# Performance work log

Hardware: AMD Instinct MI355X
Metric: run time of the kernel (lower is better)

Reference implementation:

```python
import jax, jax.numpy as jnp
import numpy as np

B, N, F_IN, H, OUT = 64, 1024, 195, 128, 64
K1, K2 = N // 2, N // 4  # ceil(0.5*N), ceil(0.5*K1)
EPS = 1e-5


def setup_inputs() -> dict:
    key = jax.random.key(0)
    ks = jax.random.split(key, 16)
    rn = lambda k, s: jax.random.normal(k, s, dtype=jnp.float32) * 0.1
    inp = {
        "input": jax.random.normal(ks[0], (B, N, F_IN), dtype=jnp.float32),
        # SAGEConv1 (195->128): lin_l (neighbors, w/ bias), lin_r (root, no bias)
        "W1l": rn(ks[1], (H, F_IN)), "b1l": jnp.zeros((H,), jnp.float32),
        "W1r": rn(ks[2], (H, F_IN)),
        # SAGPooling1 GNN = GraphConv(128->1): lin_rel (sum aggr, w/ bias), lin_root (no bias)
        "Wp1_rel": rn(ks[3], (1, H)), "bp1_rel": jnp.zeros((1,), jnp.float32),
        "Wp1_root": rn(ks[4], (1, H)),
        # SAGEConv2 (128->64)
        "W2l": rn(ks[5], (OUT, H)), "b2l": jnp.zeros((OUT,), jnp.float32),
        "W2r": rn(ks[6], (OUT, H)),
        # SAGPooling2 GNN = GraphConv(64->1)
        "Wp2_rel": rn(ks[7], (1, OUT)), "bp2_rel": jnp.zeros((1,), jnp.float32),
        "Wp2_root": rn(ks[8], (1, OUT)),
        # MLP head
        "fc1_w": rn(ks[9], (512, OUT)), "fc1_b": jnp.zeros((512,), jnp.float32),
        "bn1_g": jnp.ones((512,), jnp.float32), "bn1_b": jnp.zeros((512,), jnp.float32),
        "bn1_m": jnp.zeros((512,), jnp.float32), "bn1_v": jnp.ones((512,), jnp.float32),
        "fc2_w": rn(ks[10], (256, 512)), "fc2_b": jnp.zeros((256,), jnp.float32),
        "bn2_g": jnp.ones((256,), jnp.float32), "bn2_b": jnp.zeros((256,), jnp.float32),
        "bn2_m": jnp.zeros((256,), jnp.float32), "bn2_v": jnp.ones((256,), jnp.float32),
        "fc3_w": rn(ks[11], (2, 256)), "fc3_b": jnp.zeros((2,), jnp.float32),
    }
    return inp


def _corr_adj(x):
    # Pearson corrcoef over rows of x [B,N,F] -> boolean adjacency [B,N,N] (corr > 0.5)
    xc = x - x.mean(axis=-1, keepdims=True)
    cov = jnp.einsum("bnf,bmf->bnm", xc, xc)
    d = jnp.sqrt(jnp.clip(jnp.einsum("bnnf->bn", cov[..., None] * 0 + 0) + jnp.diagonal(cov, axis1=1, axis2=2), 1e-12))
    corr = cov / (d[:, :, None] * d[:, None, :])
    return (corr > 0.5).astype(x.dtype)  # symmetric, includes self-loops


def _sage(x, A, Wl, bl, Wr):
    # PyG SAGEConv: lin_l(mean_{j in N(i)} x_j) + lin_r(x_i)
    deg = A.sum(axis=-1, keepdims=True)
    agg = jnp.einsum("bnm,bmf->bnf", A, x) / jnp.maximum(deg, 1.0)
    return jnp.einsum("bnf,hf->bnh", agg, Wl) + bl + jnp.einsum("bnf,hf->bnh", x, Wr)


def _sagpool(x, A, Wrel, brel, Wroot, k):
    # score via GraphConv (sum aggr): lin_rel(sum_j x_j) + lin_root(x_i)
    agg = jnp.einsum("bnm,bmf->bnf", A, x)
    score = (jnp.einsum("bnf,of->bno", agg, Wrel) + brel
             + jnp.einsum("bnf,of->bno", x, Wroot))[..., 0]  # [B,N]
    top_s, idx = jax.lax.top_k(score, k)  # per-graph top-k nodes
    x_new = jnp.take_along_axis(x, idx[:, :, None], axis=1) * jnp.tanh(top_s)[:, :, None]
    A_new = jnp.take_along_axis(A, idx[:, :, None], axis=1)
    A_new = jnp.take_along_axis(A_new, idx[:, None, :], axis=2)
    return x_new, A_new


def _bn_eval(x, g, b, m, v):
    return g * (x - m) * jax.lax.rsqrt(v + EPS) + b


def reference(input, W1l, b1l, W1r, Wp1_rel, bp1_rel, Wp1_root,
              W2l, b2l, W2r, Wp2_rel, bp2_rel, Wp2_root,
              fc1_w, fc1_b, bn1_g, bn1_b, bn1_m, bn1_v,
              fc2_w, fc2_b, bn2_g, bn2_b, bn2_m, bn2_v,
              fc3_w, fc3_b):
    A = _corr_adj(input)                                   # [B,N,N]
    x = jax.nn.relu(_sage(input, A, W1l, b1l, W1r))        # [B,N,128]
    x, A = _sagpool(x, A, Wp1_rel, bp1_rel, Wp1_root, K1)  # [B,K1,128]
    x = jax.nn.relu(_sage(x, A, W2l, b2l, W2r))            # [B,K1,64]
    x, A = _sagpool(x, A, Wp2_rel, bp2_rel, Wp2_root, K2)  # [B,K2,64]
    x = x.mean(axis=1)                                     # global mean pool -> [B,64]
    x = _bn_eval(jax.nn.relu(x @ fc1_w.T + fc1_b), bn1_g, bn1_b, bn1_m, bn1_v)
    x = _bn_eval(jax.nn.relu(x @ fc2_w.T + fc2_b), bn2_g, bn2_b, bn2_m, bn2_v)
    x = x @ fc3_w.T + fc3_b
    return jax.nn.softmax(x, axis=1)
```

## Files before the change

### kernel.cpp

```cpp
#include <hip/hip_runtime.h>
#include <cstdint>


typedef __bf16 bf16x8 __attribute__((ext_vector_type(8)));
typedef float  floatx4 __attribute__((ext_vector_type(4)));

#define MFMA_BF16(a, b, c) __builtin_amdgcn_mfma_f32_16x16x32_bf16((a), (b), (c), 0, 0, 0)

static constexpr int BATCH = 64, NNODE = 1024, FIN = 195, FPAD = 224;
static constexpr int HD = 128, OD = 64, KP1 = 512, KP2 = 256;

static constexpr size_t OFF_GHI   = 0;
static constexpr size_t OFF_GLO   = 8388608;
static constexpr size_t OFF_A1B   = 16777216;
static constexpr size_t OFF_YR2   = 18874368;
static constexpr size_t OFF_X2    = 35651584;
static constexpr size_t OFF_XHI   = 0;
static constexpr size_t OFF_XLO   = 29360128;
static constexpr size_t OFF_ABITS = 58720256;
static constexpr size_t OFF_X1    = 67108864;
static constexpr size_t OFF_P1    = 100663296;
static constexpr size_t OFF_Q1    = OFF_P1 + 262144;
static constexpr size_t OFF_S1    = OFF_Q1 + 262144;
static constexpr size_t OFF_IDX1  = OFF_S1 + 262144;
static constexpr size_t OFF_GATE1 = OFF_IDX1 + 131072;
static constexpr size_t OFF_P2    = OFF_GATE1 + 131072;
static constexpr size_t OFF_Q2    = OFF_P2 + 131072;
static constexpr size_t OFF_S2    = OFF_Q2 + 131072;
static constexpr size_t OFF_IDX2  = OFF_S2 + 131072;
static constexpr size_t OFF_GATE2 = OFF_IDX2 + 65536;
static constexpr size_t OFF_W1HI  = OFF_GATE2 + 65536;
static constexpr size_t OFF_W1LO  = OFF_W1HI + 114688;
static constexpr size_t OFF_W2HI  = OFF_W1LO + 114688;
static constexpr size_t OFF_W2LO  = OFF_W2HI + 32768;
static constexpr size_t OFF_XHAT  = 102760448;
static constexpr size_t OFF_YR1   = 102760448;

__global__ __launch_bounds__(256) void prep_pack_kernel(
    const float* __restrict__ x, __bf16* __restrict__ xhi,
    __bf16* __restrict__ xlo, __bf16* __restrict__ xhat,
    const float* __restrict__ W1l, const float* __restrict__ W1r,
    __bf16* __restrict__ hi1, __bf16* __restrict__ lo1,
    const float* __restrict__ W2l, const float* __restrict__ W2r,
    __bf16* __restrict__ hi2, __bf16* __restrict__ lo2) {
  int bid = blockIdx.x;
  if (bid < 16384) {
    int row  = bid * 4 + (threadIdx.x >> 6);
    int lane = threadIdx.x & 63;
    const float* xr = x + (long)row * FIN;
    int k0 = lane * 4;
    float v[4];
#pragma unroll
    for (int i = 0; i < 4; ++i) v[i] = (k0 + i < FIN) ? xr[k0 + i] : 0.f;
    float s = v[0] + v[1] + v[2] + v[3];
#pragma unroll
    for (int o = 32; o; o >>= 1) s += __shfl_xor(s, o);
    float mean = s * (1.f / (float)FIN);
    float c[4], ss = 0.f;
#pragma unroll
    for (int i = 0; i < 4; ++i) {
      c[i] = (k0 + i < FIN) ? (v[i] - mean) : 0.f;
      ss += c[i] * c[i];
    }
#pragma unroll
    for (int o = 32; o; o >>= 1) ss += __shfl_xor(ss, o);
    float inv = rsqrtf(fmaxf(ss, 1e-12f));
    if (k0 < FPAD) {
      __bf16 hi4[4], lo4[4], hat4[4];
#pragma unroll
      for (int i = 0; i < 4; ++i) {
        float xv = (k0 + i < FIN) ? v[i] : 0.f;
        __bf16 h = (__bf16)xv;
        hi4[i] = h;
        lo4[i] = (__bf16)(xv - (float)h);
        hat4[i] = (__bf16)(c[i] * inv);
      }
      long base = (long)row * FPAD + k0;
      *(uint2*)&xhi[base]  = *(const uint2*)hi4;
      *(uint2*)&xlo[base]  = *(const uint2*)lo4;
      *(uint2*)&xhat[base] = *(const uint2*)hat4;
    }
  } else if (bid < 16384 + 224) {
    int idx = (bid - 16384) * 256 + threadIdx.x;
    int h = idx / FPAD, k = idx % FPAD;
    float v = 0.f;
    if (k < FIN) v = (h < HD) ? W1l[h * FIN + k] : W1r[(h - HD) * FIN + k];
    __bf16 a = (__bf16)v;
    hi1[idx] = a;
    lo1[idx] = (__bf16)(v - (float)a);
  } else {
    int idx = (bid - 16384 - 224) * 256 + threadIdx.x;
    int h = idx / HD, k = idx % HD;
    float v = (h < OD) ? W2l[h * HD + k] : W2r[(h - OD) * HD + k];
    __bf16 a = (__bf16)v;
    hi2[idx] = a;
    lo2[idx] = (__bf16)(v - (float)a);
  }
}

static constexpr int CK = 40;
__global__ __launch_bounds__(256) void corr_kernel(
    const __bf16* __restrict__ xhat, unsigned short* __restrict__ Abits) {
  __shared__ __align__(16) __bf16 sI[128 * CK];
  __shared__ __align__(16) __bf16 sJ[128 * CK];
  int bid = blockIdx.x;
  int xcd = bid & 7;
  int m = bid >> 3;
  int b = xcd + ((m & 7) << 3);
  int rem = m >> 3, bi = 0;
  while (rem >= 8 - bi) { rem -= 8 - bi; ++bi; }
  int bj = bi + rem;
  int i0 = bi * 128, j0 = bj * 128;
  const __bf16* Xb = xhat + (long)b * NNODE * FPAD;
  int lane = threadIdx.x & 63, wave = threadIdx.x >> 6;
  int wi = (wave >> 1) * 64, wj = (wave & 1) * 64;
  int lr = lane & 15, lk = (lane >> 4) * 8;
  int strow = threadIdx.x & 127;
  int stc = (threadIdx.x >> 7) * 8;
  floatx4 zero = {0.f, 0.f, 0.f, 0.f};
  floatx4 acc[4][4];
#pragma unroll
  for (int i = 0; i < 4; ++i)
#pragma unroll
    for (int j = 0; j < 4; ++j) acc[i][j] = zero;
  for (int kk = 0; kk < 7; ++kk) {
    int k0 = kk * 32;
    __syncthreads();
    {
      const __bf16* gI = Xb + (long)(i0 + strow) * FPAD + k0;
      const __bf16* gJ = Xb + (long)(j0 + strow) * FPAD + k0;
      *(uint4*)&sI[strow * CK + stc]      = *(const uint4*)(gI + stc);
      *(uint4*)&sI[strow * CK + stc + 16] = *(const uint4*)(gI + stc + 16);
      *(uint4*)&sJ[strow * CK + stc]      = *(const uint4*)(gJ + stc);
      *(uint4*)&sJ[strow * CK + stc + 16] = *(const uint4*)(gJ + stc + 16);
    }
    __syncthreads();
    bf16x8 af[4], bf[4];
#pragma unroll
    for (int t = 0; t < 4; ++t) {
      af[t] = *(const bf16x8*)&sI[(wi + t * 16 + lr) * CK + lk];
      bf[t] = *(const bf16x8*)&sJ[(wj + t * 16 + lr) * CK + lk];
    }
#pragma unroll
    for (int ti = 0; ti < 4; ++ti)
#pragma unroll
      for (int tj = 0; tj < 4; ++tj)
        acc[ti][tj] = MFMA_BF16(af[ti], bf[tj], acc[ti][tj]);
  }
#pragma unroll
  for (int ti = 0; ti < 4; ++ti)
#pragma unroll
    for (int tj = 0; tj < 4; ++tj) {
      floatx4 a = acc[ti][tj];
      unsigned long long m0 = __ballot(a[0] > 0.5f);
      unsigned long long m1 = __ballot(a[1] > 0.5f);
      unsigned long long m2 = __ballot(a[2] > 0.5f);
      unsigned long long m3 = __ballot(a[3] > 0.5f);
      if (lane < 16) {
        unsigned long long mm = (lane & 2) ? ((lane & 1) ? m3 : m2)
                                           : ((lane & 1) ? m1 : m0);
        unsigned short piece = (unsigned short)(mm >> ((lane >> 2) * 16));
        int grow = i0 + wi + ti * 16 + lane;
        int gcol = (j0 + wj + tj * 16) >> 4;
        Abits[((long)b * NNODE + grow) * 64 + gcol] = piece;
      }
    }
}

template <int K, int NCOL>
__global__ __launch_bounds__(256, 2) void gemm_split_kernel(
    const __bf16* __restrict__ Ahi, const __bf16* __restrict__ Alo,
    const __bf16* __restrict__ Bhi, const __bf16* __restrict__ Blo,
    float* __restrict__ C, int mblocks,
    unsigned long long* __restrict__ A64, int ntrans) {
  constexpr int ldc = NCOL * 128;
  int bid = blockIdx.x;
  if (bid >= mblocks * NCOL) {
    int t = bid - mblocks * NCOL;
    if (t >= ntrans) return;
    int b = t / 28, pi = t % 28;
    int rem = pi, rb = 1;
    while (rem >= rb) { rem -= rb; ++rb; }
    int cb = rem;
    int wave = threadIdx.x >> 6, lane = threadIdx.x & 63;
    int dr = rb * 2 + (wave >> 1);
    int dc = cb * 2 + (wave & 1);
    long base = (long)b * NNODE;
    unsigned long long xv = A64[(base + dc * 64 + lane) * 16 + dr];
    const unsigned long long M1  = 0x5555555555555555ULL;
    const unsigned long long M2  = 0x3333333333333333ULL;
    const unsigned long long M4  = 0x0F0F0F0F0F0F0F0FULL;
    const unsigned long long M8  = 0x00FF00FF00FF00FFULL;
    const unsigned long long M16 = 0x0000FFFF0000FFFFULL;
    const unsigned long long M32 = 0x00000000FFFFFFFFULL;
#define TSTEP(Kk, M)                                                      \
    {                                                                     \
      unsigned long long y = __shfl_xor(xv, Kk);                          \
      xv = ((lane & Kk) == 0) ? ((xv & (M)) | ((y & (M)) << Kk))          \
                              : ((xv & ~(M)) | ((y & ~(M)) >> Kk));       \
    }
    TSTEP(1, M1) TSTEP(2, M2) TSTEP(4, M4) TSTEP(8, M8) TSTEP(16, M16) TSTEP(32, M32)
#undef TSTEP
    A64[(base + dr * 64 + lane) * 16 + dc] = xv;
    return;
  }
  int mrow, col;
  if (NCOL == 2) {
    int xcd = bid & 7;
    int q = bid >> 3;
    col = q & 1;
    mrow = (xcd << 6) + (q >> 1);
  } else {
    mrow = bid;
    col = 0;
  }
  long row0 = (long)mrow * 128;
  int col0 = col * 128;
  int lane = threadIdx.x & 63, wave = threadIdx.x >> 6;
  int wi = (wave >> 1) * 64, wj = (wave & 1) * 64;
  int lr = lane & 15, lk = (lane >> 4) * 8;
  const __bf16* pAh = Ahi + (row0 + wi + lr) * (long)K + lk;
  const __bf16* pAl = Alo + (row0 + wi + lr) * (long)K + lk;
  const __bf16* pBh = Bhi + (long)(col0 + wj + lr) * K + lk;
  const __bf16* pBl = Blo + (long)(col0 + wj + lr) * K + lk;
  floatx4 zero = {0.f, 0.f, 0.f, 0.f};
  floatx4 acc[4][4];
#pragma unroll
  for (int i = 0; i < 4; ++i)
#pragma unroll
    for (int j = 0; j < 4; ++j) acc[i][j] = zero;
#pragma unroll
  for (int kk = 0; kk < (K >> 5); ++kk) {
    int k0 = kk * 32;
    bf16x8 ah[4], al[4], bh[4], bl[4];
#pragma unroll
    for (int t = 0; t < 4; ++t) {
      ah[t] = *(const bf16x8*)(pAh + (long)t * 16 * K + k0);
      al[t] = *(const bf16x8*)(pAl + (long)t * 16 * K + k0);
      bh[t] = *(const bf16x8*)(pBh + (long)t * 16 * K + k0);
      bl[t] = *(const bf16x8*)(pBl + (long)t * 16 * K + k0);
    }
#pragma unroll
    for (int tj = 0; tj < 4; ++tj)
#pragma unroll
      for (int ti = 0; ti < 4; ++ti) {
        acc[ti][tj] = MFMA_BF16(ah[ti], bh[tj], acc[ti][tj]);
        acc[ti][tj] = MFMA_BF16(ah[ti], bl[tj], acc[ti][tj]);
        acc[ti][tj] = MFMA_BF16(al[ti], bh[tj], acc[ti][tj]);
      }
  }
#pragma unroll
  for (int ti = 0; ti < 4; ++ti)
#pragma unroll
    for (int tj = 0; tj < 4; ++tj)
#pragma unroll
      for (int rr = 0; rr < 4; ++rr) {
        long grow = row0 + wi + ti * 16 + (lane >> 4) * 4 + rr;
        int gcol = col0 + wj + tj * 16 + (lane & 15);
        C[grow * ldc + gcol] = acc[ti][tj][rr];
      }
}

__global__ __launch_bounds__(256) void sage1_kernel(
    const unsigned int* __restrict__ Abits32, const float* __restrict__ YR1,
    const float* __restrict__ b1l, const float* __restrict__ Wrel,
    const float* __restrict__ Wroot, float* __restrict__ x1,
    float* __restrict__ p1, float* __restrict__ q1) {
  int half = threadIdx.x >> 7;
  int node = blockIdx.x * 2 + half;
  int b = node >> 10;
  int h = threadIdx.x & 127;
  __shared__ int list[2][1024];
  __shared__ int s_deg[2];
  __shared__ float redp[2][2], redq[2][2];
  if (h < 32) {
    unsigned int word = Abits32[(long)node * 32 + h];
    int cnt = __popc(word);
    int off = cnt;
#pragma unroll
    for (int o = 1; o < 32; o <<= 1) {
      int v = __shfl_up(off, o);
      if (h >= o) off += v;
    }
    off -= cnt;
    if (h == 31) s_deg[half] = off + cnt;
    int basei = h * 32;
    while (word) {
      int t = __ffs(word) - 1;
      word &= word - 1;
      list[half][off++] = basei + t;
    }
  }
  __syncthreads();
  int deg = s_deg[half];
  long ybase = (long)(b << 10) * 256;
  float accv = 0.f;
  for (int d = 0; d < deg; ++d)
    accv += YR1[ybase + (long)list[half][d] * 256 + h];
  float R = YR1[(long)node * 256 + 128 + h];
  float v = accv / (float)(deg < 1 ? 1 : deg) + b1l[h] + R;
  v = fmaxf(v, 0.f);
  x1[(long)node * 128 + h] = v;
  float pv = v * Wrel[h], qv = v * Wroot[h];
#pragma unroll
  for (int o = 32; o; o >>= 1) { pv += __shfl_xor(pv, o); qv += __shfl_xor(qv, o); }
  int wv = h >> 6, lane = h & 63;
  if (lane == 0) { redp[half][wv] = pv; redq[half][wv] = qv; }
  __syncthreads();
  if (h == 0) {
    p1[node] = redp[half][0] + redp[half][1];
    q1[node] = redq[half][0] + redq[half][1];
  }
}

__global__ __launch_bounds__(256) void score_kernel(
    const unsigned int* __restrict__ bits32, const float* __restrict__ p,
    const float* __restrict__ q, const float* __restrict__ brel,
    float* __restrict__ score, int nwords, int rpb_shift) {
  int row = blockIdx.x * 4 + (threadIdx.x >> 6);
  int lane = threadIdx.x & 63;
  int b = row >> rpb_shift;
  const unsigned int* wptr = bits32 + (long)row * nwords;
  const float* pb = p + ((long)b << rpb_shift);
  float s = 0.f;
  if (lane < nwords) {
    unsigned int word = wptr[lane];
    while (word) {
      int t = __ffs(word) - 1;
      word &= word - 1;
      s += pb[lane * 32 + t];
    }
  }
#pragma unroll
  for (int o = 32; o; o >>= 1) s += __shfl_xor(s, o);
  if (lane == 0) score[row] = s + q[row] + brel[0];
}

__global__ void topk_kernel(const float* __restrict__ score, int n, int k,
                            int* __restrict__ idx_out, float* __restrict__ gate_out) {
  int b = blockIdx.x, tid = threadIdx.x;
  float s = score[b * n + tid];
  unsigned int fb = __float_as_uint(s);
  unsigned int key = (fb & 0x80000000u) ? ~fb : (fb | 0x80000000u);
  __shared__ int hist[256];
  __shared__ unsigned int sh_prefix;
  __shared__ int sh_target, cnt_gt, cnt_eq, outpos;
  if (tid == 0) { sh_prefix = 0; sh_target = k; cnt_gt = 0; cnt_eq = 0; outpos = 0; }
  for (int shift = 24; shift >= 0; shift -= 8) {
    if (tid < 256) hist[tid] = 0;
    __syncthreads();
    unsigned int prefix = sh_prefix;
    bool inset = (shift == 24) || ((key >> (shift + 8)) == (prefix >> (shift + 8)));
    if (inset) atomicAdd(&hist[(key >> shift) & 255], 1);
    __syncthreads();
    if (tid < 64) {
      int lane = tid;
      int bb0 = hist[255 - 4 * lane];
      int bb1 = hist[254 - 4 * lane];
      int bb2 = hist[253 - 4 * lane];
      int bb3 = hist[252 - 4 * lane];
      int c0 = bb0, c1 = c0 + bb1, c2 = c1 + bb2, c3 = c2 + bb3;
      int incl = c3;
#pragma unroll
      for (int o = 1; o < 64; o <<= 1) {
        int v = __shfl_up(incl, o);
        if (lane >= o) incl += v;
      }
      int excl = incl - c3;
      int target = sh_target;
      int cum[4] = {excl + c0, excl + c1, excl + c2, excl + c3};
      int prev = excl;
#pragma unroll
      for (int i = 0; i < 4; ++i) {
        if (cum[i] >= target && prev < target) {
          int bin = 255 - (4 * lane + i);
          sh_prefix = prefix | ((unsigned int)bin << shift);
          sh_target = target - prev;
        }
        prev = cum[i];
      }
    }
    __syncthreads();
  }
  unsigned int T = sh_prefix;
  if (key > T) atomicAdd(&cnt_gt, 1);
  __syncthreads();
  int E = k - cnt_gt;
  bool sel = (key > T);
  if (!sel && key == T) sel = (atomicAdd(&cnt_eq, 1) < E);
  if (sel) {
    int posn = atomicAdd(&outpos, 1);
    idx_out[b * k + posn] = tid;
    gate_out[b * k + posn] = tanhf(s);
  }
}

__global__ __launch_bounds__(256) void gather_kernel(
    const float* __restrict__ x1, const int* __restrict__ idx,
    const float* __restrict__ gate, __bf16* __restrict__ ghi,
    __bf16* __restrict__ glo, const unsigned int* __restrict__ Abits32,
    unsigned long long* __restrict__ A1bits) {
  int bid = blockIdx.x;
  if (bid < 16384) {
    long e = (long)bid * 256 + threadIdx.x;
    int h = (int)(e & 127);
    int i = (int)((e >> 7) & 511);
    int b = (int)(e >> 16);
    int srow = idx[(b << 9) + i];
    float v = x1[((long)(b << 10) + srow) * 128 + h] * gate[(b << 9) + i];
    __bf16 a = (__bf16)v;
    ghi[e] = a;
    glo[e] = (__bf16)(v - (float)a);
  } else {
    int gi = (bid - 16384) * 4 + (threadIdx.x >> 6);
    int lane = threadIdx.x & 63;
    int b = gi >> 9;
    int srow = idx[gi];
    const unsigned int* src = Abits32 + ((long)(b << 10) + srow) * 32;
    const int* idxb = idx + (b << 9);
#pragma unroll
    for (int t = 0; t < 8; ++t) {
      int cj = idxb[t * 64 + lane];
      int bit = (src[cj >> 5] >> (cj & 31)) & 1;
      unsigned long long m = __ballot(bit);
      if (lane == 0) A1bits[(long)gi * 8 + t] = m;
    }
  }
}

__global__ __launch_bounds__(256) void sage2_kernel(
    const unsigned int* __restrict__ A1b32, const float* __restrict__ YR2,
    const float* __restrict__ b2l, const float* __restrict__ Wrel,
    const float* __restrict__ Wroot, float* __restrict__ x2,
    float* __restrict__ p2, float* __restrict__ q2) {
  int qw = threadIdx.x >> 6;
  int row = blockIdx.x * 4 + qw;
  int b = row >> 9;
  int h = threadIdx.x & 63;
  __shared__ int list[4][512];
  __shared__ int s_deg[4];
  if (h < 16) {
    unsigned int word = A1b32[(long)row * 16 + h];
    int cnt = __popc(word);
    int off = cnt;
#pragma unroll
    for (int o = 1; o < 16; o <<= 1) {
      int v = __shfl_up(off, o);
      if (h >= o) off += v;
    }
    off -= cnt;
    if (h == 15) s_deg[qw] = off + cnt;
    int basei = h * 32;
    while (word) {
      int t = __ffs(word) - 1;
      word &= word - 1;
      list[qw][off++] = basei + t;
    }
  }
  __syncthreads();
  int deg = s_deg[qw];
  long ybase = (long)(b << 9) * 128;
  float accv = 0.f;
  for (int d = 0; d < deg; ++d)
    accv += YR2[ybase + (long)list[qw][d] * 128 + h];
  float R = YR2[(long)row * 128 + 64 + h];
  float v = fmaxf(accv / (float)(deg < 1 ? 1 : deg) + b2l[h] + R, 0.f);
  x2[(long)row * 64 + h] = v;
  float pv = v * Wrel[h], qv = v * Wroot[h];
#pragma unroll
  for (int o = 32; o; o >>= 1) { pv += __shfl_xor(pv, o); qv += __shfl_xor(qv, o); }
  if (h == 0) { p2[row] = pv; q2[row] = qv; }
}

__global__ __launch_bounds__(512) void head_kernel(
    const float* __restrict__ x2, const int* __restrict__ idx2,
    const float* __restrict__ gate2, const float* __restrict__ fc1_w,
    const float* __restrict__ fc1_b, const float* __restrict__ g1,
    const float* __restrict__ bb1, const float* __restrict__ m1,
    const float* __restrict__ v1, const float* __restrict__ fc2_w,
    const float* __restrict__ fc2_b, const float* __restrict__ g2,
    const float* __restrict__ bb2, const float* __restrict__ m2,
    const float* __restrict__ v2, const float* __restrict__ fc3_w,
    const float* __restrict__ fc3_b, float* __restrict__ out) {
  int b = blockIdx.x, tid = threadIdx.x;
  __shared__ float part[8][64];
  __shared__ float pooled[64];
  __shared__ float h1[512];
  __shared__ float h2[256];
  __shared__ float zz[2];
  int h = tid & 63, grp = tid >> 6;
  float s = 0.f;
  for (int i = grp * 32; i < grp * 32 + 32; ++i) {
    int si = idx2[(b << 8) + i];
    s += x2[((long)(b << 9) + si) * 64 + h] * gate2[(b << 8) + i];
  }
  part[grp][h] = s;
  __syncthreads();
  if (tid < 64) {
    float t = 0.f;
#pragma unroll
    for (int g = 0; g < 8; ++g) t += part[g][tid];
    pooled[tid] = t * (1.f / 256.f);
  }
  __syncthreads();
  {
    float z = fc1_b[tid];
    for (int j = 0; j < 64; ++j) z += pooled[j] * fc1_w[tid * 64 + j];
    z = fmaxf(z, 0.f);
    h1[tid] = g1[tid] * (z - m1[tid]) * rsqrtf(v1[tid] + 1e-5f) + bb1[tid];
  }
  __syncthreads();
  if (tid < 256) {
    float z = fc2_b[tid];
    for (int j = 0; j < 512; ++j) z += h1[j] * fc2_w[tid * 512 + j];
    z = fmaxf(z, 0.f);
    h2[tid] = g2[tid] * (z - m2[tid]) * rsqrtf(v2[tid] + 1e-5f) + bb2[tid];
  }
  __syncthreads();
  if (tid < 2) {
    float z = fc3_b[tid];
    for (int j = 0; j < 256; ++j) z += h2[j] * fc3_w[tid * 256 + j];
    zz[tid] = z;
  }
  __syncthreads();
  if (tid == 0) {
    float mx = fmaxf(zz[0], zz[1]);
    float e0 = expf(zz[0] - mx), e1 = expf(zz[1] - mx);
    float inv = 1.f / (e0 + e1);
    out[b * 2 + 0] = e0 * inv;
    out[b * 2 + 1] = e1 * inv;
  }
}

extern "C" void kernel_launch(void* const* d_in, const int* in_sizes, int n_in,
                              void* d_out, int out_size, void* d_ws, size_t ws_size,
                              hipStream_t stream) {
  (void)in_sizes; (void)n_in; (void)out_size; (void)ws_size;
  const float* input   = (const float*)d_in[0];
  const float* W1l     = (const float*)d_in[1];
  const float* b1l     = (const float*)d_in[2];
  const float* W1r     = (const float*)d_in[3];
  const float* Wp1_rel = (const float*)d_in[4];
  const float* bp1_rel = (const float*)d_in[5];
  const float* Wp1_root= (const float*)d_in[6];
  const float* W2l     = (const float*)d_in[7];
  const float* b2l     = (const float*)d_in[8];
  const float* W2r     = (const float*)d_in[9];
  const float* Wp2_rel = (const float*)d_in[10];
  const float* bp2_rel = (const float*)d_in[11];
  const float* Wp2_root= (const float*)d_in[12];
  const float* fc1_w   = (const float*)d_in[13];
  const float* fc1_b   = (const float*)d_in[14];
  const float* bn1_g   = (const float*)d_in[15];
  const float* bn1_b   = (const float*)d_in[16];
  const float* bn1_m   = (const float*)d_in[17];
  const float* bn1_v   = (const float*)d_in[18];
  const float* fc2_w   = (const float*)d_in[19];
  const float* fc2_b   = (const float*)d_in[20];
  const float* bn2_g   = (const float*)d_in[21];
  const float* bn2_b   = (const float*)d_in[22];
  const float* bn2_m   = (const float*)d_in[23];
  const float* bn2_v   = (const float*)d_in[24];
  const float* fc3_w   = (const float*)d_in[25];
  const float* fc3_b   = (const float*)d_in[26];

  char* ws = (char*)d_ws;
  __bf16* xhi   = (__bf16*)(ws + OFF_XHI);
  __bf16* xlo   = (__bf16*)(ws + OFF_XLO);
  __bf16* xhat  = (__bf16*)(ws + OFF_XHAT);
  unsigned short* Abits = (unsigned short*)(ws + OFF_ABITS);
  const unsigned int* Abits32 = (const unsigned int*)(ws + OFF_ABITS);
  unsigned long long* A64 = (unsigned long long*)(ws + OFF_ABITS);
  float* YR1    = (float*)(ws + OFF_YR1);
  float* x1     = (float*)(ws + OFF_X1);
  float* p1     = (float*)(ws + OFF_P1);
  float* q1     = (float*)(ws + OFF_Q1);
  float* s1     = (float*)(ws + OFF_S1);
  int*   idx1   = (int*)(ws + OFF_IDX1);
  float* gate1  = (float*)(ws + OFF_GATE1);
  float* p2     = (float*)(ws + OFF_P2);
  float* q2     = (float*)(ws + OFF_Q2);
  float* s2     = (float*)(ws + OFF_S2);
  int*   idx2   = (int*)(ws + OFF_IDX2);
  float* gate2  = (float*)(ws + OFF_GATE2);
  __bf16* w1hi  = (__bf16*)(ws + OFF_W1HI);
  __bf16* w1lo  = (__bf16*)(ws + OFF_W1LO);
  __bf16* w2hi  = (__bf16*)(ws + OFF_W2HI);
  __bf16* w2lo  = (__bf16*)(ws + OFF_W2LO);
  __bf16* ghi   = (__bf16*)(ws + OFF_GHI);
  __bf16* glo   = (__bf16*)(ws + OFF_GLO);
  unsigned long long* A1bits = (unsigned long long*)(ws + OFF_A1B);
  const unsigned int* A1b32  = (const unsigned int*)(ws + OFF_A1B);
  float* YR2    = (float*)(ws + OFF_YR2);
  float* x2     = (float*)(ws + OFF_X2);
  float* out    = (float*)d_out;

  prep_pack_kernel<<<16672, 256, 0, stream>>>(input, xhi, xlo, xhat,
                                              W1l, W1r, w1hi, w1lo,
                                              W2l, W2r, w2hi, w2lo);
  corr_kernel<<<2304, 256, 0, stream>>>(xhat, Abits);
  gemm_split_kernel<224, 2><<<1024 + 1792, 256, 0, stream>>>(
      xhi, xlo, w1hi, w1lo, YR1, 512, A64, 1792);
  sage1_kernel<<<32768, 256, 0, stream>>>(Abits32, YR1, b1l, Wp1_rel, Wp1_root, x1, p1, q1);
  score_kernel<<<16384, 256, 0, stream>>>(Abits32, p1, q1, bp1_rel, s1, 32, 10);
  topk_kernel<<<64, 1024, 0, stream>>>(s1, 1024, KP1, idx1, gate1);
  gather_kernel<<<24576, 256, 0, stream>>>(x1, idx1, gate1, ghi, glo, Abits32, A1bits);
  gemm_split_kernel<128, 1><<<256, 256, 0, stream>>>(
      ghi, glo, w2hi, w2lo, YR2, 256, nullptr, 0);
  sage2_kernel<<<8192, 256, 0, stream>>>(A1b32, YR2, b2l, Wp2_rel, Wp2_root, x2, p2, q2);
  score_kernel<<<8192, 256, 0, stream>>>(A1b32, p2, q2, bp2_rel, s2, 16, 9);
  topk_kernel<<<64, 512, 0, stream>>>(s2, 512, KP2, idx2, gate2);
  head_kernel<<<64, 512, 0, stream>>>(x2, idx2, gate2, fc1_w, fc1_b, bn1_g, bn1_b,
                                      bn1_m, bn1_v, fc2_w, fc2_b, bn2_g, bn2_b,
                                      bn2_m, bn2_v, fc3_w, fc3_b, out);
}
```

Baseline: 376.4 us.

## Fuse score with top-k and head, split GEMM tiles across 512 threads

Score computation is merged into the top-k kernel, where each thread computes its own row's score serially. For the second pooling stage, score, top-k and the MLP head run in one kernel, with indices and gates kept in shared memory. This removes three launches and the global score, idx2 and gate2 round-trips. The split-bf16 GEMM now uses 512-thread blocks with 32-row wave tiles to raise parallelism and cut per-thread registers. The cost is that score computation now runs on only 64 blocks with serial per-thread loops, which risks poor occupancy for the 1024-node stage.

```diff
diff --git a/kernel.cpp b/kernel.cpp
--- a/kernel.cpp
+++ b/kernel.cpp
@@ -21,15 +21,11 @@
 static constexpr size_t OFF_X1    = 67108864;
 static constexpr size_t OFF_P1    = 100663296;
 static constexpr size_t OFF_Q1    = OFF_P1 + 262144;
-static constexpr size_t OFF_S1    = OFF_Q1 + 262144;
-static constexpr size_t OFF_IDX1  = OFF_S1 + 262144;
+static constexpr size_t OFF_IDX1  = OFF_Q1 + 262144;
 static constexpr size_t OFF_GATE1 = OFF_IDX1 + 131072;
 static constexpr size_t OFF_P2    = OFF_GATE1 + 131072;
 static constexpr size_t OFF_Q2    = OFF_P2 + 131072;
-static constexpr size_t OFF_S2    = OFF_Q2 + 131072;
-static constexpr size_t OFF_IDX2  = OFF_S2 + 131072;
-static constexpr size_t OFF_GATE2 = OFF_IDX2 + 65536;
-static constexpr size_t OFF_W1HI  = OFF_GATE2 + 65536;
+static constexpr size_t OFF_W1HI  = OFF_Q2 + 131072;
 static constexpr size_t OFF_W1LO  = OFF_W1HI + 114688;
 static constexpr size_t OFF_W2HI  = OFF_W1LO + 114688;
 static constexpr size_t OFF_W2LO  = OFF_W2HI + 32768;
@@ -168,7 +164,7 @@
 }
 
 template <int K, int NCOL>
-__global__ __launch_bounds__(256, 2) void gemm_split_kernel(
+__global__ __launch_bounds__(512, 2) void gemm_split_kernel(
     const __bf16* __restrict__ Ahi, const __bf16* __restrict__ Alo,
     const __bf16* __restrict__ Bhi, const __bf16* __restrict__ Blo,
     float* __restrict__ C, int mblocks,
@@ -177,7 +173,7 @@
   int bid = blockIdx.x;
   if (bid >= mblocks * NCOL) {
     int t = bid - mblocks * NCOL;
-    if (t >= ntrans) return;
+    if (t >= ntrans || threadIdx.x >= 256) return;
     int b = t / 28, pi = t % 28;
     int rem = pi, rb = 1;
     while (rem >= rb) { rem -= rb; ++rb; }
@@ -217,40 +213,43 @@
   long row0 = (long)mrow * 128;
   int col0 = col * 128;
   int lane = threadIdx.x & 63, wave = threadIdx.x >> 6;
-  int wi = (wave >> 1) * 64, wj = (wave & 1) * 64;
+  int wi = (wave >> 1) * 32, wj = (wave & 1) * 64;
   int lr = lane & 15, lk = (lane >> 4) * 8;
   const __bf16* pAh = Ahi + (row0 + wi + lr) * (long)K + lk;
   const __bf16* pAl = Alo + (row0 + wi + lr) * (long)K + lk;
   const __bf16* pBh = Bhi + (long)(col0 + wj + lr) * K + lk;
   const __bf16* pBl = Blo + (long)(col0 + wj + lr) * K + lk;
   floatx4 zero = {0.f, 0.f, 0.f, 0.f};
-  floatx4 acc[4][4];
-#pragma unroll
-  for (int i = 0; i < 4; ++i)
+  floatx4 acc[2][4];
+#pragma unroll
+  for (int i = 0; i < 2; ++i)
 #pragma unroll
     for (int j = 0; j < 4; ++j) acc[i][j] = zero;
 #pragma unroll
   for (int kk = 0; kk < (K >> 5); ++kk) {
     int k0 = kk * 32;
-    bf16x8 ah[4], al[4], bh[4], bl[4];
-#pragma unroll
-    for (int t = 0; t < 4; ++t) {
+    bf16x8 ah[2], al[2], bh[4], bl[4];
+#pragma unroll
+    for (int t = 0; t < 2; ++t) {
       ah[t] = *(const bf16x8*)(pAh + (long)t * 16 * K + k0);
       al[t] = *(const bf16x8*)(pAl + (long)t * 16 * K + k0);
+    }
+#pragma unroll
+    for (int t = 0; t < 4; ++t) {
       bh[t] = *(const bf16x8*)(pBh + (long)t * 16 * K + k0);
       bl[t] = *(const bf16x8*)(pBl + (long)t * 16 * K + k0);
     }
 #pragma unroll
     for (int tj = 0; tj < 4; ++tj)
 #pragma unroll
-      for (int ti = 0; ti < 4; ++ti) {
+      for (int ti = 0; ti < 2; ++ti) {
         acc[ti][tj] = MFMA_BF16(ah[ti], bh[tj], acc[ti][tj]);
         acc[ti][tj] = MFMA_BF16(ah[ti], bl[tj], acc[ti][tj]);
         acc[ti][tj] = MFMA_BF16(al[ti], bh[tj], acc[ti][tj]);
       }
   }
 #pragma unroll
-  for (int ti = 0; ti < 4; ++ti)
+  for (int ti = 0; ti < 2; ++ti)
 #pragma unroll
     for (int tj = 0; tj < 4; ++tj)
 #pragma unroll
@@ -313,33 +312,26 @@
   }
 }
 
-__global__ __launch_bounds__(256) void score_kernel(
-    const unsigned int* __restrict__ bits32, const float* __restrict__ p,
-    const float* __restrict__ q, const float* __restrict__ brel,
-    float* __restrict__ score, int nwords, int rpb_shift) {
-  int row = blockIdx.x * 4 + (threadIdx.x >> 6);
-  int lane = threadIdx.x & 63;
-  int b = row >> rpb_shift;
+__global__ void scoretopk_kernel(const unsigned int* __restrict__ bits32,
+                                 const float* __restrict__ p,
+                                 const float* __restrict__ q,
+                                 const float* __restrict__ brel,
+                                 int* __restrict__ idx_out,
+                                 float* __restrict__ gate_out,
+                                 int nwords, int rpb_shift, int k) {
+  int b = blockIdx.x, tid = threadIdx.x;
+  int row = (b << rpb_shift) + tid;
   const unsigned int* wptr = bits32 + (long)row * nwords;
   const float* pb = p + ((long)b << rpb_shift);
-  float s = 0.f;
-  if (lane < nwords) {
-    unsigned int word = wptr[lane];
+  float s = q[row] + brel[0];
+  for (int w = 0; w < nwords; ++w) {
+    unsigned int word = wptr[w];
     while (word) {
       int t = __ffs(word) - 1;
       word &= word - 1;
-      s += pb[lane * 32 + t];
-    }
-  }
-#pragma unroll
-  for (int o = 32; o; o >>= 1) s += __shfl_xor(s, o);
-  if (lane == 0) score[row] = s + q[row] + brel[0];
-}
-
-__global__ void topk_kernel(const float* __restrict__ score, int n, int k,
-                            int* __restrict__ idx_out, float* __restrict__ gate_out) {
-  int b = blockIdx.x, tid = threadIdx.x;
-  float s = score[b * n + tid];
+      s += pb[w * 32 + t];
+    }
+  }
   unsigned int fb = __float_as_uint(s);
   unsigned int key = (fb & 0x80000000u) ? ~fb : (fb | 0x80000000u);
   __shared__ int hist[256];
@@ -472,9 +464,10 @@
   if (h == 0) { p2[row] = pv; q2[row] = qv; }
 }
 
-__global__ __launch_bounds__(512) void head_kernel(
-    const float* __restrict__ x2, const int* __restrict__ idx2,
-    const float* __restrict__ gate2, const float* __restrict__ fc1_w,
+__global__ __launch_bounds__(512) void scoretopk_head_kernel(
+    const unsigned int* __restrict__ A1b32, const float* __restrict__ p2,
+    const float* __restrict__ q2, const float* __restrict__ brel,
+    const float* __restrict__ x2, const float* __restrict__ fc1_w,
     const float* __restrict__ fc1_b, const float* __restrict__ g1,
     const float* __restrict__ bb1, const float* __restrict__ m1,
     const float* __restrict__ v1, const float* __restrict__ fc2_w,
@@ -483,18 +476,87 @@
     const float* __restrict__ v2, const float* __restrict__ fc3_w,
     const float* __restrict__ fc3_b, float* __restrict__ out) {
   int b = blockIdx.x, tid = threadIdx.x;
+  int row = (b << 9) + tid;
+  const unsigned int* wptr = A1b32 + (long)row * 16;
+  const float* pb = p2 + ((long)b << 9);
+  float s = q2[row] + brel[0];
+  for (int w = 0; w < 16; ++w) {
+    unsigned int word = wptr[w];
+    while (word) {
+      int t = __ffs(word) - 1;
+      word &= word - 1;
+      s += pb[w * 32 + t];
+    }
+  }
+  constexpr int k = KP2;
+  unsigned int fb = __float_as_uint(s);
+  unsigned int key = (fb & 0x80000000u) ? ~fb : (fb | 0x80000000u);
+  __shared__ int hist[256];
+  __shared__ int idx2s[256];
+  __shared__ float gate2s[256];
+  __shared__ unsigned int sh_prefix;
+  __shared__ int sh_target, cnt_gt, cnt_eq, outpos;
+  if (tid == 0) { sh_prefix = 0; sh_target = k; cnt_gt = 0; cnt_eq = 0; outpos = 0; }
+  for (int shift = 24; shift >= 0; shift -= 8) {
+    if (tid < 256) hist[tid] = 0;
+    __syncthreads();
+    unsigned int prefix = sh_prefix;
+    bool inset = (shift == 24) || ((key >> (shift + 8)) == (prefix >> (shift + 8)));
+    if (inset) atomicAdd(&hist[(key >> shift) & 255], 1);
+    __syncthreads();
+    if (tid < 64) {
+      int lane = tid;
+      int bb0 = hist[255 - 4 * lane];
+      int bb1 = hist[254 - 4 * lane];
+      int bb2 = hist[253 - 4 * lane];
+      int bb3 = hist[252 - 4 * lane];
+      int c0 = bb0, c1 = c0 + bb1, c2 = c1 + bb2, c3 = c2 + bb3;
+      int incl = c3;
+#pragma unroll
+      for (int o = 1; o < 64; o <<= 1) {
+        int v = __shfl_up(incl, o);
+        if (lane >= o) incl += v;
+      }
+      int excl = incl - c3;
+      int target = sh_target;
+      int cum[4] = {excl + c0, excl + c1, excl + c2, excl + c3};
+      int prev = excl;
+#pragma unroll
+      for (int i = 0; i < 4; ++i) {
+        if (cum[i] >= target && prev < target) {
+          int bin = 255 - (4 * lane + i);
+          sh_prefix = prefix | ((unsigned int)bin << shift);
+          sh_target = target - prev;
+        }
+        prev = cum[i];
+      }
+    }
+    __syncthreads();
+  }
+  unsigned int T = sh_prefix;
+  if (key > T) atomicAdd(&cnt_gt, 1);
+  __syncthreads();
+  int E = k - cnt_gt;
+  bool sel = (key > T);
+  if (!sel && key == T) sel = (atomicAdd(&cnt_eq, 1) < E);
+  if (sel) {
+    int posn = atomicAdd(&outpos, 1);
+    idx2s[posn] = tid;
+    gate2s[posn] = tanhf(s);
+  }
+  __syncthreads();
   __shared__ float part[8][64];
   __shared__ float pooled[64];
   __shared__ float h1[512];
   __shared__ float h2[256];
   __shared__ float zz[2];
   int h = tid & 63, grp = tid >> 6;
-  float s = 0.f;
+  float sp = 0.f;
   for (int i = grp * 32; i < grp * 32 + 32; ++i) {
-    int si = idx2[(b << 8) + i];
-    s += x2[((long)(b << 9) + si) * 64 + h] * gate2[(b << 8) + i];
-  }
-  part[grp][h] = s;
+    int si = idx2s[i];
+    sp += x2[((long)(b << 9) + si) * 64 + h] * gate2s[i];
+  }
+  part[grp][h] = sp;
   __syncthreads();
   if (tid < 64) {
     float t = 0.f;
@@ -575,14 +637,10 @@
   float* x1     = (float*)(ws + OFF_X1);
   float* p1     = (float*)(ws + OFF_P1);
   float* q1     = (float*)(ws + OFF_Q1);
-  float* s1     = (float*)(ws + OFF_S1);
   int*   idx1   = (int*)(ws + OFF_IDX1);
   float* gate1  = (float*)(ws + OFF_GATE1);
   float* p2     = (float*)(ws + OFF_P2);
   float* q2     = (float*)(ws + OFF_Q2);
-  float* s2     = (float*)(ws + OFF_S2);
-  int*   idx2   = (int*)(ws + OFF_IDX2);
-  float* gate2  = (float*)(ws + OFF_GATE2);
   __bf16* w1hi  = (__bf16*)(ws + OFF_W1HI);
   __bf16* w1lo  = (__bf16*)(ws + OFF_W1LO);
   __bf16* w2hi  = (__bf16*)(ws + OFF_W2HI);
@@ -599,18 +657,17 @@
                                               W1l, W1r, w1hi, w1lo,
                                               W2l, W2r, w2hi, w2lo);
   corr_kernel<<<2304, 256, 0, stream>>>(xhat, Abits);
-  gemm_split_kernel<224, 2><<<1024 + 1792, 256, 0, stream>>>(
+  gemm_split_kernel<224, 2><<<1024 + 1792, 512, 0, stream>>>(
       xhi, xlo, w1hi, w1lo, YR1, 512, A64, 1792);
   sage1_kernel<<<32768, 256, 0, stream>>>(Abits32, YR1, b1l, Wp1_rel, Wp1_root, x1, p1, q1);
-  score_kernel<<<16384, 256, 0, stream>>>(Abits32, p1, q1, bp1_rel, s1, 32, 10);
-  topk_kernel<<<64, 1024, 0, stream>>>(s1, 1024, KP1, idx1, gate1);
+  scoretopk_kernel<<<64, 1024, 0, stream>>>(Abits32, p1, q1, bp1_rel, idx1, gate1,
+                                            32, 10, KP1);
   gather_kernel<<<24576, 256, 0, stream>>>(x1, idx1, gate1, ghi, glo, Abits32, A1bits);
-  gemm_split_kernel<128, 1><<<256, 256, 0, stream>>>(
+  gemm_split_kernel<128, 1><<<256, 512, 0, stream>>>(
       ghi, glo, w2hi, w2lo, YR2, 256, nullptr, 0);
   sage2_kernel<<<8192, 256, 0, stream>>>(A1b32, YR2, b2l, Wp2_rel, Wp2_root, x2, p2, q2);
-  score_kernel<<<8192, 256, 0, stream>>>(A1b32, p2, q2, bp2_rel, s2, 16, 9);
-  topk_kernel<<<64, 512, 0, stream>>>(s2, 512, KP2, idx2, gate2);
-  head_kernel<<<64, 512, 0, stream>>>(x2, idx2, gate2, fc1_w, fc1_b, bn1_g, bn1_b,
-                                      bn1_m, bn1_v, fc2_w, fc2_b, bn2_g, bn2_b,
-                                      bn2_m, bn2_v, fc3_w, fc3_b, out);
-}
+  scoretopk_head_kernel<<<64, 512, 0, stream>>>(A1b32, p2, q2, bp2_rel, x2,
+                                                fc1_w, fc1_b, bn1_g, bn1_b, bn1_m, bn1_v,
+                                                fc2_w, fc2_b, bn2_g, bn2_b, bn2_m, bn2_v,
+                                                fc3_w, fc3_b, out);
+}
```

Result: slower. 389.9 us (+3.6%).
